# Kernel optimization log

Measured on AMD Instinct MI355X. Metric: run time of the kernel, lower is better.

Reference implementation:

```python
import jax, jax.numpy as jnp
import numpy as np

H, F, E, TOPK = 2048, 8192, 8, 2
B, S = 2, 256


def setup_inputs() -> dict:
    key = jax.random.key(0)
    kx, kg, k1, k2, k3 = jax.random.split(key, 5)
    scale = 0.02
    return {
        "x": jax.random.normal(kx, (B, S, H), dtype=jnp.float32),
        "Wg": jax.random.normal(kg, (H, E), dtype=jnp.float32) * scale,
        "W1": jax.random.normal(k1, (E, H, F), dtype=jnp.float32) * scale,
        "W2": jax.random.normal(k2, (E, F, H), dtype=jnp.float32) * scale,
        "W3": jax.random.normal(k3, (E, H, F), dtype=jnp.float32) * scale,
    }


def reference(x, Wg, W1, W2, W3):
    B_, S_, H_ = x.shape
    xf = x.reshape(-1, H_)                      # [T, H]
    T = xf.shape[0]

    # Router: gate logits -> softmax -> top-k, renormalize selected weights.
    logits = xf @ Wg                            # [T, E]
    probs = jax.nn.softmax(logits, axis=-1)
    topw, topi = jax.lax.top_k(probs, TOPK)     # [T, K]
    topw = topw / jnp.sum(topw, axis=-1, keepdims=True)

    # Combine matrix: combine[t, e] = routing weight of expert e for token t (0 if unselected).
    combine = jnp.zeros((T, E), dtype=x.dtype).at[jnp.arange(T)[:, None], topi].add(topw)

    # Per-expert gated MLP (dense over experts; zeros in `combine` drop unselected experts).
    h1 = jnp.einsum("th,ehf->etf", xf, W1)      # [E, T, F]
    h3 = jnp.einsum("th,ehf->etf", xf, W3)      # [E, T, F]
    h = jax.nn.relu(h1) * h3                    # gated activation
    ye = jnp.einsum("etf,efh->eth", h, W2)      # [E, T, H]

    out = jnp.einsum("eth,te->th", ye, combine) # scatter-add combine
    return out.reshape(B_, S_, H_)
```

## Files before the change

kernel.cpp:

```cpp
#include <hip/hip_runtime.h>
#include <hip/hip_bf16.h>


#define HDIM 2048
#define FDIM 8192
#define NEXP 8
#define NTOK 512
#define MAXT 512

typedef __attribute__((ext_vector_type(8))) short short8;
typedef __attribute__((ext_vector_type(4))) float f32x4;
typedef unsigned int u32;
typedef unsigned short u16;

__device__ __forceinline__ unsigned cvtpk(float lo, float hi) {
    unsigned r;
    asm("v_cvt_pk_bf16_f32 %0, %1, %2" : "=v"(r) : "v"(lo), "v"(hi));
    return r;
}
__device__ __forceinline__ unsigned f2bf1(float f) {
    unsigned u = __builtin_bit_cast(unsigned, f);
    return (u + 0x7FFFu + ((u >> 16) & 1u)) >> 16;
}
__device__ __forceinline__ void gload16(const void* g, void* l) {
    __builtin_amdgcn_global_load_lds((const __attribute__((address_space(1))) u32*)g,
                                     (__attribute__((address_space(3))) u32*)l, 16, 0, 0);
}
#define SBAR() __builtin_amdgcn_sched_barrier(0)

__global__ void moe_router(const float* __restrict__ x, const float* __restrict__ Wg,
                           int* __restrict__ counts, int* __restrict__ tok_id,
                           float* __restrict__ tok_w) {
    const int t = blockIdx.x;
    const int lane = threadIdx.x;
    const float* xr = x + (size_t)t * HDIM;
    float acc[8];
    #pragma unroll
    for (int e = 0; e < 8; ++e) acc[e] = 0.f;
    #pragma unroll 4
    for (int i = 0; i < HDIM / 64; ++i) {
        int h = lane + i * 64;
        float xv = xr[h];
        const float4* wr = (const float4*)(Wg + (size_t)h * 8);
        float4 wa = wr[0], wb = wr[1];
        acc[0] += xv * wa.x; acc[1] += xv * wa.y; acc[2] += xv * wa.z; acc[3] += xv * wa.w;
        acc[4] += xv * wb.x; acc[5] += xv * wb.y; acc[6] += xv * wb.z; acc[7] += xv * wb.w;
    }
    #pragma unroll
    for (int off = 32; off >= 1; off >>= 1) {
        #pragma unroll
        for (int e = 0; e < 8; ++e) acc[e] += __shfl_xor(acc[e], off);
    }
    if (lane == 0) {
        int e0 = 0;
        #pragma unroll
        for (int e = 1; e < 8; ++e) if (acc[e] > acc[e0]) e0 = e;
        int e1 = (e0 == 0) ? 1 : 0;
        #pragma unroll
        for (int e = 0; e < 8; ++e) if (e != e0 && acc[e] > acc[e1]) e1 = e;
        float w0 = 1.f / (1.f + __expf(acc[e1] - acc[e0]));
        float w1 = 1.f - w0;
        int s0 = atomicAdd(&counts[e0], 1);
        tok_id[e0 * MAXT + s0] = t; tok_w[e0 * MAXT + s0] = w0;
        int s1 = atomicAdd(&counts[e1], 1);
        tok_id[e1 * MAXT + s1] = t; tok_w[e1 * MAXT + s1] = w1;
    }
}

__global__ void moe_scan(const int* __restrict__ counts, int* __restrict__ offsets) {
    if (threadIdx.x == 0) {
        int a = 0;
        for (int e = 0; e < NEXP; ++e) { offsets[e] = a; a += counts[e]; }
    }
}

__global__ void moe_xcvt(const float* __restrict__ x, u16* __restrict__ xbf) {
    const int i = (blockIdx.x * 256 + threadIdx.x) * 8;
    float4 a = *(const float4*)(x + i);
    float4 b = *(const float4*)(x + i + 4);
    uint4 q;
    q.x = cvtpk(a.x, a.y); q.y = cvtpk(a.z, a.w);
    q.z = cvtpk(b.x, b.y); q.w = cvtpk(b.z, b.w);
    *(uint4*)(xbf + i) = q;
}

__device__ __forceinline__ short8 bfrag(const float* sB, int kbase, int nsw) {
    const float* p = sB + kbase * 64 + nsw;
    float f[8];
    #pragma unroll
    for (int j = 0; j < 8; ++j) f[j] = p[j * 64];
    uint4 q;
    q.x = cvtpk(f[0], f[1]); q.y = cvtpk(f[2], f[3]);
    q.z = cvtpk(f[4], f[5]); q.w = cvtpk(f[6], f[7]);
    return __builtin_bit_cast(short8, q);
}

__global__ __launch_bounds__(256, 2)
void moe_gemm1(const u16* __restrict__ xbf, const float* __restrict__ W1,
               const float* __restrict__ W3, const int* __restrict__ counts,
               const int* __restrict__ offsets, const int* __restrict__ tok_id,
               u16* __restrict__ hbuf) {
    const int nt = blockIdx.x, mt = blockIdx.y, e = blockIdx.z;
    const int cnt = counts[e];
    if (mt * 128 >= cnt) return;
    const int n0 = nt * 64;
    const int tid = threadIdx.x;
    const int w = tid >> 6, l = tid & 63;

    __shared__ __align__(16) u16 sApad[2][128 * 40];
    __shared__ __align__(16) float sB1[2][2048];
    __shared__ __align__(16) float sB3[2][2048];

    const int arow = tid >> 1;
    const int akc = (tid & 1) * 16;
    const int aslot = mt * 128 + arow;
    const int atok = tok_id[e * MAXT + (aslot < cnt ? aslot : cnt - 1)];
    const u16* areg_src = xbf + (size_t)atok * HDIM + akc;

    const int kr = l >> 4, c4 = l & 15;
    const size_t wstride = (size_t)HDIM * FDIM;
    const float* b1p[2]; const float* b3p[2];
    #pragma unroll
    for (int i = 0; i < 2; ++i) {
        int krow = i * 16 + w * 4 + kr;
        size_t off = (size_t)e * wstride + (size_t)krow * FDIM + n0 +
                     (size_t)((c4 ^ (((krow >> 3) & 1) << 2)) * 4);
        b1p[i] = W1 + off; b3p[i] = W3 + off;
    }

    const int wr = (w >> 1) * 64, wc = (w & 1) * 32;
    const int lr = l & 15, lg = l >> 4;
    const int lk = lg * 8;
    const int g1 = lg & 1;

    f32x4 acc1[4][2], acc3[4][2];
    #pragma unroll
    for (int mi = 0; mi < 4; ++mi)
        #pragma unroll
        for (int ni = 0; ni < 2; ++ni) { acc1[mi][ni] = (f32x4)0.f; acc3[mi][ni] = (f32x4)0.f; }

    uint4 a0, a1;
    #define ALOAD1(kt) { const u16* s_ = areg_src + (kt) * 32;                 \
                         a0 = *(const uint4*)s_; a1 = *(const uint4*)(s_ + 8); }
    #define AWRITE1(buf) { *(uint4*)&sApad[buf][arow * 40 + akc] = a0;         \
                           *(uint4*)&sApad[buf][arow * 40 + akc + 8] = a1; }
    #define BSTAGE1(buf, kt)                                                   \
        _Pragma("unroll")                                                      \
        for (int i = 0; i < 2; ++i) {                                          \
            gload16(b1p[i] + (size_t)(kt) * 32 * FDIM, &sB1[buf][(i * 16 + w * 4) * 64]); \
            gload16(b3p[i] + (size_t)(kt) * 32 * FDIM, &sB3[buf][(i * 16 + w * 4) * 64]); \
        }

    ALOAD1(0);
    SBAR();
    BSTAGE1(0, 0);
    SBAR();
    for (int kt = 0; kt < HDIM / 32; ++kt) {
        const int cur = kt & 1;
        asm volatile("s_waitcnt vmcnt(4)" ::: "memory");
        SBAR();
        AWRITE1(cur);
        SBAR();
        if (kt + 1 < HDIM / 32) {
            ALOAD1(kt + 1);
            SBAR();
            BSTAGE1(cur ^ 1, kt + 1);
            SBAR();
            asm volatile("s_waitcnt vmcnt(6) lgkmcnt(0)" ::: "memory");
        } else {
            asm volatile("s_waitcnt vmcnt(0) lgkmcnt(0)" ::: "memory");
        }
        SBAR();
        __builtin_amdgcn_s_barrier();
        SBAR();
        short8 a[4];
        #pragma unroll
        for (int mi = 0; mi < 4; ++mi)
            a[mi] = *(const short8*)&sApad[cur][(wr + mi * 16 + lr) * 40 + lk];
        #pragma unroll
        for (int ni = 0; ni < 2; ++ni) {
            const int nsw = (wc + ni * 16 + lr) ^ (g1 << 4);
            short8 b1 = bfrag(sB1[cur], lk, nsw);
            short8 b3 = bfrag(sB3[cur], lk, nsw);
            #pragma unroll
            for (int mi = 0; mi < 4; ++mi) {
                acc1[mi][ni] = __builtin_amdgcn_mfma_f32_16x16x32_bf16(a[mi], b1, acc1[mi][ni], 0, 0, 0);
                acc3[mi][ni] = __builtin_amdgcn_mfma_f32_16x16x32_bf16(a[mi], b3, acc3[mi][ni], 0, 0, 0);
            }
        }
        SBAR();
        __builtin_amdgcn_s_barrier();
        SBAR();
    }
    const int hbase = offsets[e] + mt * 128;
    #pragma unroll
    for (int mi = 0; mi < 4; ++mi)
        #pragma unroll
        for (int ni = 0; ni < 2; ++ni)
            #pragma unroll
            for (int r = 0; r < 4; ++r) {
                int rl = wr + mi * 16 + (l >> 4) * 4 + r;
                int sl = mt * 128 + rl;
                if (sl < cnt) {
                    float v1 = acc1[mi][ni][r];
                    v1 = v1 > 0.f ? v1 : 0.f;
                    float hv = v1 * acc3[mi][ni][r];
                    hbuf[(size_t)(hbase + rl) * FDIM + (n0 + wc + ni * 16 + lr)] =
                        (u16)f2bf1(hv);
                }
            }
}

__global__ __launch_bounds__(256, 2)
void moe_gemm2(const u16* __restrict__ hbuf, const float* __restrict__ W2,
               const int* __restrict__ counts, const int* __restrict__ offsets,
               const int* __restrict__ tok_id, const float* __restrict__ tok_w,
               float* __restrict__ out) {
    const int nt = blockIdx.x, e = blockIdx.z;
    const int mt = blockIdx.y & 3, ksp = blockIdx.y >> 2;
    const int cnt = counts[e];
    if (mt * 128 >= cnt) return;
    const int n0 = nt * 64;
    const int tid = threadIdx.x;
    const int w = tid >> 6, l = tid & 63;

    __shared__ __align__(16) u16 sApad[2][128 * 40];
    __shared__ __align__(16) float sB[2][2048];

    const int arow = tid >> 1;
    const int akc = (tid & 1) * 16;
    const int hrow = offsets[e] + mt * 128 + arow;
    const u16* areg_src = hbuf + (size_t)hrow * FDIM + ksp * 2048 + akc;

    const int kr = l >> 4, c4 = l & 15;
    const float* b2p[2];
    #pragma unroll
    for (int i = 0; i < 2; ++i) {
        int krow = i * 16 + w * 4 + kr;
        b2p[i] = W2 + (size_t)e * ((size_t)FDIM * HDIM) + (size_t)(ksp * 2048 + krow) * HDIM +
                 n0 + (size_t)((c4 ^ (((krow >> 3) & 1) << 2)) * 4);
    }

    const int wr = (w >> 1) * 64, wc = (w & 1) * 32;
    const int lr = l & 15, lg = l >> 4;
    const int lk = lg * 8;
    const int g1 = lg & 1;

    f32x4 acc[4][2];
    #pragma unroll
    for (int mi = 0; mi < 4; ++mi)
        #pragma unroll
        for (int ni = 0; ni < 2; ++ni) acc[mi][ni] = (f32x4)0.f;

    uint4 a0, a1;
    #define ALOAD2(kt) { const u16* s_ = areg_src + (kt) * 32;                 \
                         a0 = *(const uint4*)s_; a1 = *(const uint4*)(s_ + 8); }
    #define AWRITE2(buf) { *(uint4*)&sApad[buf][arow * 40 + akc] = a0;         \
                           *(uint4*)&sApad[buf][arow * 40 + akc + 8] = a1; }
    #define BSTAGE2(buf, kt)                                                   \
        _Pragma("unroll")                                                      \
        for (int i = 0; i < 2; ++i)                                            \
            gload16(b2p[i] + (size_t)(kt) * 32 * HDIM, &sB[buf][(i * 16 + w * 4) * 64]);

    ALOAD2(0);
    SBAR();
    BSTAGE2(0, 0);
    SBAR();
    for (int kt = 0; kt < 64; ++kt) {
        const int cur = kt & 1;
        asm volatile("s_waitcnt vmcnt(2)" ::: "memory");
        SBAR();
        AWRITE2(cur);
        SBAR();
        if (kt + 1 < 64) {
            ALOAD2(kt + 1);
            SBAR();
            BSTAGE2(cur ^ 1, kt + 1);
            SBAR();
            asm volatile("s_waitcnt vmcnt(4) lgkmcnt(0)" ::: "memory");
        } else {
            asm volatile("s_waitcnt vmcnt(0) lgkmcnt(0)" ::: "memory");
        }
        SBAR();
        __builtin_amdgcn_s_barrier();
        SBAR();
        short8 a[4];
        #pragma unroll
        for (int mi = 0; mi < 4; ++mi)
            a[mi] = *(const short8*)&sApad[cur][(wr + mi * 16 + lr) * 40 + lk];
        #pragma unroll
        for (int ni = 0; ni < 2; ++ni) {
            const int nsw = (wc + ni * 16 + lr) ^ (g1 << 4);
            short8 b = bfrag(sB[cur], lk, nsw);
            #pragma unroll
            for (int mi = 0; mi < 4; ++mi)
                acc[mi][ni] = __builtin_amdgcn_mfma_f32_16x16x32_bf16(a[mi], b, acc[mi][ni], 0, 0, 0);
        }
        SBAR();
        __builtin_amdgcn_s_barrier();
        SBAR();
    }
    #pragma unroll
    for (int mi = 0; mi < 4; ++mi)
        #pragma unroll
        for (int ni = 0; ni < 2; ++ni)
            #pragma unroll
            for (int r = 0; r < 4; ++r) {
                int rl = wr + mi * 16 + (l >> 4) * 4 + r;
                int sl = mt * 128 + rl;
                if (sl < cnt) {
                    int tk = tok_id[e * MAXT + sl];
                    float wgt = tok_w[e * MAXT + sl];
                    atomicAdd(&out[(size_t)tk * HDIM + (n0 + wc + ni * 16 + lr)],
                              wgt * acc[mi][ni][r]);
                }
            }
}

extern "C" void kernel_launch(void* const* d_in, const int* in_sizes, int n_in,
                              void* d_out, int out_size, void* d_ws, size_t ws_size,
                              hipStream_t stream) {
    const float* x  = (const float*)d_in[0];
    const float* Wg = (const float*)d_in[1];
    const float* W1 = (const float*)d_in[2];
    const float* W2 = (const float*)d_in[3];
    const float* W3 = (const float*)d_in[4];
    float* out = (float*)d_out;

    char* ws = (char*)d_ws;
    int*   counts  = (int*)(ws + 0);
    int*   offsets = (int*)(ws + 32);
    int*   tok_id  = (int*)(ws + 64);
    float* tok_w   = (float*)(ws + 64 + NEXP * MAXT * 4);
    u16*   xbf     = (u16*)(ws + 65536);
    u16*   hbuf    = (u16*)(ws + 65536 + (size_t)NTOK * HDIM * 2);

    hipMemsetAsync(ws, 0, 64, stream);
    hipMemsetAsync(d_out, 0, (size_t)out_size * sizeof(float), stream);

    moe_router<<<NTOK, 64, 0, stream>>>(x, Wg, counts, tok_id, tok_w);
    moe_scan<<<1, 64, 0, stream>>>(counts, offsets);
    moe_xcvt<<<NTOK * HDIM / (256 * 8), 256, 0, stream>>>(x, xbf);
    moe_gemm1<<<dim3(FDIM / 64, 4, NEXP), 256, 0, stream>>>(xbf, W1, W3, counts, offsets, tok_id, hbuf);
    moe_gemm2<<<dim3(HDIM / 64, 16, NEXP), 256, 0, stream>>>(hbuf, W2, counts, offsets, tok_id, tok_w, out);
}
```

Baseline: 523.1 us.

## Load A fragments directly to registers and triple-buffer B with deeper prefetch

Both grouped GEMM kernels stop staging the activation (A) tile through shared memory. Each lane now loads its MFMA A fragment straight from global memory into registers, double-buffered across iterations. The B weight tiles move from a two-stage to a three-stage LDS ring, prefetched two k-steps ahead, with the loop unrolled by two and explicit vmcnt waits. This removes LDS writes and reads for A and one barrier pair per step, at the cost of more VGPRs and uncoalesced per-row A loads.

```diff
diff --git a/kernel.cpp b/kernel.cpp
--- a/kernel.cpp
+++ b/kernel.cpp
@@ -107,16 +107,21 @@
     const int tid = threadIdx.x;
     const int w = tid >> 6, l = tid & 63;
 
-    __shared__ __align__(16) u16 sApad[2][128 * 40];
-    __shared__ __align__(16) float sB1[2][2048];
-    __shared__ __align__(16) float sB3[2][2048];
-
-    const int arow = tid >> 1;
-    const int akc = (tid & 1) * 16;
-    const int aslot = mt * 128 + arow;
-    const int atok = tok_id[e * MAXT + (aslot < cnt ? aslot : cnt - 1)];
-    const u16* areg_src = xbf + (size_t)atok * HDIM + akc;
-
+    __shared__ __align__(16) float sB1[3 * 2048];
+    __shared__ __align__(16) float sB3[3 * 2048];
+
+    const int wr = (w >> 1) * 64, wc = (w & 1) * 32;
+    const int lr = l & 15, lg = l >> 4;
+    const int lk = lg * 8;
+    const int g1 = lg & 1;
+
+    const u16* abase[4];
+    #pragma unroll
+    for (int mi = 0; mi < 4; ++mi) {
+        int slot = mt * 128 + wr + mi * 16 + lr;
+        int tok = tok_id[e * MAXT + (slot < cnt ? slot : cnt - 1)];
+        abase[mi] = xbf + (size_t)tok * HDIM + lk;
+    }
     const int kr = l >> 4, c4 = l & 15;
     const size_t wstride = (size_t)HDIM * FDIM;
     const float* b1p[2]; const float* b3p[2];
@@ -128,70 +133,68 @@
         b1p[i] = W1 + off; b3p[i] = W3 + off;
     }
 
-    const int wr = (w >> 1) * 64, wc = (w & 1) * 32;
-    const int lr = l & 15, lg = l >> 4;
-    const int lk = lg * 8;
-    const int g1 = lg & 1;
-
     f32x4 acc1[4][2], acc3[4][2];
     #pragma unroll
     for (int mi = 0; mi < 4; ++mi)
         #pragma unroll
         for (int ni = 0; ni < 2; ++ni) { acc1[mi][ni] = (f32x4)0.f; acc3[mi][ni] = (f32x4)0.f; }
 
-    uint4 a0, a1;
-    #define ALOAD1(kt) { const u16* s_ = areg_src + (kt) * 32;                 \
-                         a0 = *(const uint4*)s_; a1 = *(const uint4*)(s_ + 8); }
-    #define AWRITE1(buf) { *(uint4*)&sApad[buf][arow * 40 + akc] = a0;         \
-                           *(uint4*)&sApad[buf][arow * 40 + akc + 8] = a1; }
-    #define BSTAGE1(buf, kt)                                                   \
+    uint4 afA[4], afB[4];
+    unsigned o0 = 0, o1 = 2048, o2 = 4096;
+
+    #define AISSUE1(AF, kt)                                                    \
+        _Pragma("unroll")                                                      \
+        for (int mi = 0; mi < 4; ++mi)                                         \
+            AF[mi] = *(const uint4*)(abase[mi] + (size_t)(kt) * 32);
+    #define BSTAGE1(ob, kt)                                                    \
         _Pragma("unroll")                                                      \
         for (int i = 0; i < 2; ++i) {                                          \
-            gload16(b1p[i] + (size_t)(kt) * 32 * FDIM, &sB1[buf][(i * 16 + w * 4) * 64]); \
-            gload16(b3p[i] + (size_t)(kt) * 32 * FDIM, &sB3[buf][(i * 16 + w * 4) * 64]); \
+            gload16(b1p[i] + (size_t)(kt) * 32 * FDIM, &sB1[(ob) + (i * 16 + w * 4) * 64]); \
+            gload16(b3p[i] + (size_t)(kt) * 32 * FDIM, &sB3[(ob) + (i * 16 + w * 4) * 64]); \
         }
-
-    ALOAD1(0);
-    SBAR();
-    BSTAGE1(0, 0);
-    SBAR();
-    for (int kt = 0; kt < HDIM / 32; ++kt) {
-        const int cur = kt & 1;
-        asm volatile("s_waitcnt vmcnt(4)" ::: "memory");
-        SBAR();
-        AWRITE1(cur);
-        SBAR();
-        if (kt + 1 < HDIM / 32) {
-            ALOAD1(kt + 1);
-            SBAR();
-            BSTAGE1(cur ^ 1, kt + 1);
-            SBAR();
-            asm volatile("s_waitcnt vmcnt(6) lgkmcnt(0)" ::: "memory");
-        } else {
-            asm volatile("s_waitcnt vmcnt(0) lgkmcnt(0)" ::: "memory");
+    #define MFMAP1(AF, ob)                                                     \
+        _Pragma("unroll")                                                      \
+        for (int ni = 0; ni < 2; ++ni) {                                       \
+            const int nsw = (wc + ni * 16 + lr) ^ (g1 << 4);                   \
+            short8 b1 = bfrag(sB1 + (ob), lk, nsw);                            \
+            short8 b3 = bfrag(sB3 + (ob), lk, nsw);                            \
+            _Pragma("unroll")                                                  \
+            for (int mi = 0; mi < 4; ++mi) {                                   \
+                short8 a_ = __builtin_bit_cast(short8, AF[mi]);                \
+                acc1[mi][ni] = __builtin_amdgcn_mfma_f32_16x16x32_bf16(a_, b1, acc1[mi][ni], 0, 0, 0); \
+                acc3[mi][ni] = __builtin_amdgcn_mfma_f32_16x16x32_bf16(a_, b3, acc3[mi][ni], 0, 0, 0); \
+            }                                                                  \
         }
-        SBAR();
+    #define BODY1(kt, oCur, oStg, ARD, ALD, VM)                                \
+        SBAR(); AISSUE1(ALD, (kt) + 1); SBAR();                                \
+        BSTAGE1(oStg, (kt) + 2); SBAR();                                       \
+        asm volatile("s_waitcnt vmcnt(" VM ")" ::: "memory"); SBAR();          \
+        __builtin_amdgcn_s_barrier(); SBAR();                                  \
+        MFMAP1(ARD, oCur); SBAR();                                             \
         __builtin_amdgcn_s_barrier();
-        SBAR();
-        short8 a[4];
-        #pragma unroll
-        for (int mi = 0; mi < 4; ++mi)
-            a[mi] = *(const short8*)&sApad[cur][(wr + mi * 16 + lr) * 40 + lk];
-        #pragma unroll
-        for (int ni = 0; ni < 2; ++ni) {
-            const int nsw = (wc + ni * 16 + lr) ^ (g1 << 4);
-            short8 b1 = bfrag(sB1[cur], lk, nsw);
-            short8 b3 = bfrag(sB3[cur], lk, nsw);
-            #pragma unroll
-            for (int mi = 0; mi < 4; ++mi) {
-                acc1[mi][ni] = __builtin_amdgcn_mfma_f32_16x16x32_bf16(a[mi], b1, acc1[mi][ni], 0, 0, 0);
-                acc3[mi][ni] = __builtin_amdgcn_mfma_f32_16x16x32_bf16(a[mi], b3, acc3[mi][ni], 0, 0, 0);
-            }
-        }
-        SBAR();
-        __builtin_amdgcn_s_barrier();
-        SBAR();
-    }
+
+    BSTAGE1(o0, 0); SBAR();
+    AISSUE1(afA, 0); SBAR();
+    BSTAGE1(o1, 1);
+    for (int kt = 0; kt < 62; kt += 2) {
+        BODY1(kt, o0, o2, afA, afB, "12");
+        BODY1(kt + 1, o1, o0, afB, afA, "12");
+        unsigned t_ = o0; o0 = o2; o2 = o1; o1 = t_;
+    }
+    SBAR(); AISSUE1(afB, 63); SBAR();
+    asm volatile("s_waitcnt vmcnt(8)" ::: "memory"); SBAR();
+    __builtin_amdgcn_s_barrier(); SBAR();
+    MFMAP1(afA, o0); SBAR();
+    __builtin_amdgcn_s_barrier(); SBAR();
+    asm volatile("s_waitcnt vmcnt(0)" ::: "memory"); SBAR();
+    __builtin_amdgcn_s_barrier(); SBAR();
+    MFMAP1(afB, o1); SBAR();
+
+    #undef AISSUE1
+    #undef BSTAGE1
+    #undef MFMAP1
+    #undef BODY1
+
     const int hbase = offsets[e] + mt * 128;
     #pragma unroll
     for (int mi = 0; mi < 4; ++mi)
@@ -224,14 +227,19 @@
     const int tid = threadIdx.x;
     const int w = tid >> 6, l = tid & 63;
 
-    __shared__ __align__(16) u16 sApad[2][128 * 40];
-    __shared__ __align__(16) float sB[2][2048];
-
-    const int arow = tid >> 1;
-    const int akc = (tid & 1) * 16;
-    const int hrow = offsets[e] + mt * 128 + arow;
-    const u16* areg_src = hbuf + (size_t)hrow * FDIM + ksp * 2048 + akc;
-
+    __shared__ __align__(16) float sB[3 * 2048];
+
+    const int wr = (w >> 1) * 64, wc = (w & 1) * 32;
+    const int lr = l & 15, lg = l >> 4;
+    const int lk = lg * 8;
+    const int g1 = lg & 1;
+
+    const u16* abase[4];
+    #pragma unroll
+    for (int mi = 0; mi < 4; ++mi) {
+        int hrow = offsets[e] + mt * 128 + wr + mi * 16 + lr;
+        abase[mi] = hbuf + (size_t)hrow * FDIM + ksp * 2048 + lk;
+    }
     const int kr = l >> 4, c4 = l & 15;
     const float* b2p[2];
     #pragma unroll
@@ -241,65 +249,64 @@
                  n0 + (size_t)((c4 ^ (((krow >> 3) & 1) << 2)) * 4);
     }
 
-    const int wr = (w >> 1) * 64, wc = (w & 1) * 32;
-    const int lr = l & 15, lg = l >> 4;
-    const int lk = lg * 8;
-    const int g1 = lg & 1;
-
     f32x4 acc[4][2];
     #pragma unroll
     for (int mi = 0; mi < 4; ++mi)
         #pragma unroll
         for (int ni = 0; ni < 2; ++ni) acc[mi][ni] = (f32x4)0.f;
 
-    uint4 a0, a1;
-    #define ALOAD2(kt) { const u16* s_ = areg_src + (kt) * 32;                 \
-                         a0 = *(const uint4*)s_; a1 = *(const uint4*)(s_ + 8); }
-    #define AWRITE2(buf) { *(uint4*)&sApad[buf][arow * 40 + akc] = a0;         \
-                           *(uint4*)&sApad[buf][arow * 40 + akc + 8] = a1; }
-    #define BSTAGE2(buf, kt)                                                   \
+    uint4 afA[4], afB[4];
+    unsigned o0 = 0, o1 = 2048, o2 = 4096;
+
+    #define AISSUE2(AF, kt)                                                    \
+        _Pragma("unroll")                                                      \
+        for (int mi = 0; mi < 4; ++mi)                                         \
+            AF[mi] = *(const uint4*)(abase[mi] + (size_t)(kt) * 32);
+    #define BSTAGE2(ob, kt)                                                    \
         _Pragma("unroll")                                                      \
         for (int i = 0; i < 2; ++i)                                            \
-            gload16(b2p[i] + (size_t)(kt) * 32 * HDIM, &sB[buf][(i * 16 + w * 4) * 64]);
-
-    ALOAD2(0);
-    SBAR();
-    BSTAGE2(0, 0);
-    SBAR();
-    for (int kt = 0; kt < 64; ++kt) {
-        const int cur = kt & 1;
-        asm volatile("s_waitcnt vmcnt(2)" ::: "memory");
-        SBAR();
-        AWRITE2(cur);
-        SBAR();
-        if (kt + 1 < 64) {
-            ALOAD2(kt + 1);
-            SBAR();
-            BSTAGE2(cur ^ 1, kt + 1);
-            SBAR();
-            asm volatile("s_waitcnt vmcnt(4) lgkmcnt(0)" ::: "memory");
-        } else {
-            asm volatile("s_waitcnt vmcnt(0) lgkmcnt(0)" ::: "memory");
+            gload16(b2p[i] + (size_t)(kt) * 32 * HDIM, &sB[(ob) + (i * 16 + w * 4) * 64]);
+    #define MFMAP2(AF, ob)                                                     \
+        _Pragma("unroll")                                                      \
+        for (int ni = 0; ni < 2; ++ni) {                                       \
+            const int nsw = (wc + ni * 16 + lr) ^ (g1 << 4);                   \
+            short8 b = bfrag(sB + (ob), lk, nsw);                              \
+            _Pragma("unroll")                                                  \
+            for (int mi = 0; mi < 4; ++mi) {                                   \
+                short8 a_ = __builtin_bit_cast(short8, AF[mi]);                \
+                acc[mi][ni] = __builtin_amdgcn_mfma_f32_16x16x32_bf16(a_, b, acc[mi][ni], 0, 0, 0); \
+            }                                                                  \
         }
-        SBAR();
+    #define BODY2(kt, oCur, oStg, ARD, ALD, VM)                                \
+        SBAR(); AISSUE2(ALD, (kt) + 1); SBAR();                                \
+        BSTAGE2(oStg, (kt) + 2); SBAR();                                       \
+        asm volatile("s_waitcnt vmcnt(" VM ")" ::: "memory"); SBAR();          \
+        __builtin_amdgcn_s_barrier(); SBAR();                                  \
+        MFMAP2(ARD, oCur); SBAR();                                             \
         __builtin_amdgcn_s_barrier();
-        SBAR();
-        short8 a[4];
-        #pragma unroll
-        for (int mi = 0; mi < 4; ++mi)
-            a[mi] = *(const short8*)&sApad[cur][(wr + mi * 16 + lr) * 40 + lk];
-        #pragma unroll
-        for (int ni = 0; ni < 2; ++ni) {
-            const int nsw = (wc + ni * 16 + lr) ^ (g1 << 4);
-            short8 b = bfrag(sB[cur], lk, nsw);
-            #pragma unroll
-            for (int mi = 0; mi < 4; ++mi)
-                acc[mi][ni] = __builtin_amdgcn_mfma_f32_16x16x32_bf16(a[mi], b, acc[mi][ni], 0, 0, 0);
-        }
-        SBAR();
-        __builtin_amdgcn_s_barrier();
-        SBAR();
-    }
+
+    BSTAGE2(o0, 0); SBAR();
+    AISSUE2(afA, 0); SBAR();
+    BSTAGE2(o1, 1);
+    for (int kt = 0; kt < 62; kt += 2) {
+        BODY2(kt, o0, o2, afA, afB, "8");
+        BODY2(kt + 1, o1, o0, afB, afA, "8");
+        unsigned t_ = o0; o0 = o2; o2 = o1; o1 = t_;
+    }
+    SBAR(); AISSUE2(afB, 63); SBAR();
+    asm volatile("s_waitcnt vmcnt(6)" ::: "memory"); SBAR();
+    __builtin_amdgcn_s_barrier(); SBAR();
+    MFMAP2(afA, o0); SBAR();
+    __builtin_amdgcn_s_barrier(); SBAR();
+    asm volatile("s_waitcnt vmcnt(0)" ::: "memory"); SBAR();
+    __builtin_amdgcn_s_barrier(); SBAR();
+    MFMAP2(afB, o1); SBAR();
+
+    #undef AISSUE2
+    #undef BSTAGE2
+    #undef MFMAP2
+    #undef BODY2
+
     #pragma unroll
     for (int mi = 0; mi < 4; ++mi)
         #pragma unroll
```

Result: slower. 614.9 us (+17.5%).
